# Kernel tuning notes

Hardware: AMD Instinct MI355X
Metric: run time of the kernel (lower is better)

## Reference

```python
import jax, jax.numpy as jnp
import numpy as np

B, N, D = 2, 2048, 1024
H = 16
HD = D // H  # head_dim for kq and v

def setup_inputs() -> dict:
    key = jax.random.key(0)
    ks = jax.random.split(key, 5)
    scale = 1.0 / np.sqrt(D)
    return {
        "x": jax.random.normal(ks[0], (B, N, D), dtype=jnp.float32),
        "Wq": jax.random.normal(ks[1], (D, D), dtype=jnp.float32) * scale,
        "Wk": jax.random.normal(ks[2], (D, D), dtype=jnp.float32) * scale,
        "Wv": jax.random.normal(ks[3], (D, D), dtype=jnp.float32) * scale,
        "Wo": jax.random.normal(ks[4], (D, D), dtype=jnp.float32) * scale,
        "bo": jnp.zeros((D,), dtype=jnp.float32),
    }

def reference(x, Wq, Wk, Wv, Wo, bo):
    b, n, _ = x.shape
    # projections; torch Linear computes x @ W.T
    q = (x @ Wq.T).reshape(b, n, H, HD).transpose(0, 2, 1, 3)  # [B,H,N,HD]
    k = (x @ Wk.T).reshape(b, n, H, HD).transpose(0, 2, 1, 3)
    v = (x @ Wv.T).reshape(b, n, H, HD).transpose(0, 2, 1, 3)
    scores = jnp.einsum('bhqd,bhkd->bhqk', q, k) / jnp.sqrt(jnp.asarray(HD, x.dtype))
    causal = jnp.tril(jnp.ones((n, n), dtype=bool))
    scores = jnp.where(causal, scores, jnp.asarray(-jnp.inf, scores.dtype))
    probs = jax.nn.softmax(scores, axis=-1)  # dropout p=0.0 (eval)
    out = jnp.einsum('bhqk,bhkd->bhqd', probs, v)  # [B,H,N,HD]
    out = out.transpose(0, 2, 1, 3).reshape(b, n, D)
    return out @ Wo.T + bo
```

## Files before the change

kernel.cpp:

```cpp
#include <hip/hip_runtime.h>
#include <hip/hip_bf16.h>


typedef __bf16 bf16;
typedef __bf16 bf16x2 __attribute__((ext_vector_type(2)));
typedef __bf16 bf16x4 __attribute__((ext_vector_type(4)));
typedef __bf16 bf16x8 __attribute__((ext_vector_type(8)));
typedef float f32x4 __attribute__((ext_vector_type(4)));
typedef unsigned int u32x4 __attribute__((ext_vector_type(4)));

__device__ __forceinline__ f32x4 mfma16(bf16x8 a, bf16x8 b, f32x4 c) {
    return __builtin_amdgcn_mfma_f32_16x16x32_bf16(a, b, c, 0, 0, 0);
}

__device__ __forceinline__ void gload16(const bf16* g, bf16* l) {
    __builtin_amdgcn_global_load_lds(
        (const __attribute__((address_space(1))) unsigned int*)g,
        (__attribute__((address_space(3))) unsigned int*)l, 16, 0, 0);
}

__device__ __forceinline__ unsigned pk2(float a, float b) {
    bf16x2 v;
    v[0] = (bf16)a;
    v[1] = (bf16)b;
    return __builtin_bit_cast(unsigned, v);
}

__global__ __launch_bounds__(256) void conv_kernel(
    const float* __restrict__ x, const float* __restrict__ w0,
    const float* __restrict__ w1, const float* __restrict__ w2,
    const float* __restrict__ w3, bf16* __restrict__ xb,
    bf16* __restrict__ o0, bf16* __restrict__ o1,
    bf16* __restrict__ o2, bf16* __restrict__ o3) {
    int blk = blockIdx.x;
    const float* in;
    bf16* out;
    int base;
    if (blk < 4096) {
        in = x; out = xb; base = blk;
    } else {
        int sel = (blk - 4096) >> 10;
        in = sel == 0 ? w0 : sel == 1 ? w1 : sel == 2 ? w2 : w3;
        out = sel == 0 ? o0 : sel == 1 ? o1 : sel == 2 ? o2 : o3;
        base = (blk - 4096) & 1023;
    }
    int i = (base * 256 + threadIdx.x) * 4;
    float4 v = *(const float4*)&in[i];
    bf16x4 o;
    o.x = (bf16)v.x; o.y = (bf16)v.y; o.z = (bf16)v.z; o.w = (bf16)v.w;
    *(bf16x4*)&out[i] = o;
}

template <int MODE>
__device__ __forceinline__ void gemm_body(bf16* __restrict__ sA, bf16* __restrict__ sB,
                                          const bf16* __restrict__ A,
                                          const bf16* __restrict__ B,
                                          bf16* __restrict__ Cb,
                                          float* __restrict__ Cf,
                                          const float* __restrict__ bias,
                                          float scale, int N, int K, int row0, int col0) {
    const int tid  = threadIdx.x;
    const int lane = tid & 63;
    const int wave = tid >> 6;
    const int wrow = (wave >> 1) * 64;
    const int wcol = (wave & 1) * 64;
    const int la = lane & 15, lb = lane >> 4;

    const f32x4 fzero = {0.f, 0.f, 0.f, 0.f};
    f32x4 acc[4][4];
#pragma unroll
    for (int m = 0; m < 4; ++m)
#pragma unroll
        for (int n = 0; n < 4; ++n) acc[m][n] = fzero;

    auto STAGE = [&](int k0, int buf) {
#pragma unroll
        for (int i = 0; i < 2; ++i) {
            int idx = i * 256 + tid;
            int r = idx >> 2, s = idx & 3;
            gload16(&A[(size_t)(row0 + r) * K + k0 + s * 8], &sA[buf * 4096 + idx * 8]);
            gload16(&B[(size_t)(col0 + r) * K + k0 + s * 8], &sB[buf * 4096 + idx * 8]);
        }
    };
    auto COMPUTE = [&](int buf) {
        bf16x8 af[4], bfv[4];
#pragma unroll
        for (int m = 0; m < 4; ++m)
            af[m] = *(const bf16x8*)&sA[buf * 4096 + (wrow + m * 16 + la) * 32 + lb * 8];
#pragma unroll
        for (int n = 0; n < 4; ++n)
            bfv[n] = *(const bf16x8*)&sB[buf * 4096 + (wcol + n * 16 + la) * 32 + lb * 8];
#pragma unroll
        for (int m = 0; m < 4; ++m)
#pragma unroll
            for (int n = 0; n < 4; ++n)
                acc[m][n] = mfma16(af[m], bfv[n], acc[m][n]);
    };

    STAGE(0, 0);
    __syncthreads();
    for (int k0 = 0; k0 < K; k0 += 64) {
        if (k0 + 32 < K) STAGE(k0 + 32, 1);
        COMPUTE(0);
        __syncthreads();
        if (k0 + 64 < K) STAGE(k0 + 64, 0);
        COMPUTE(1);
        __syncthreads();
    }
#pragma unroll
    for (int m = 0; m < 4; ++m)
#pragma unroll
        for (int n = 0; n < 4; ++n) {
            int col = col0 + wcol + n * 16 + la;
            if (MODE == 2) {
                int hh = col >> 6, hd = col & 63;
                int hc = hd >> 4, lav = hd & 15;
                int sp = row0 + wrow + m * 16 + lb * 4;
                int ktile = sp >> 6, k = sp & 63;
                int c = k >> 4, q = k & 15;
                size_t addr = (size_t)(ktile * 16 + hh) * 4096 +
                              (size_t)(((hc * 2 + (c >> 1)) * 16 + lav) * 32 +
                                       (q >> 2) * 8 + (c & 1) * 4);
                bf16x4 o4;
#pragma unroll
                for (int r = 0; r < 4; ++r) o4[r] = (bf16)acc[m][n][r];
                *(bf16x4*)&Cb[addr] = o4;
            } else if (MODE == 3) {
                int hh = col >> 6, hd = col & 63;
#pragma unroll
                for (int r = 0; r < 4; ++r) {
                    int row = row0 + wrow + m * 16 + lb * 4 + r;
                    int ktile = row >> 6, key = row & 63;
                    size_t addr = (size_t)(ktile * 16 + hh) * 4096 +
                                  (size_t)((((key >> 4) * 2 + (hd >> 5)) * 16 +
                                            (key & 15)) * 32 +
                                           ((hd >> 3) & 3) * 8 + (hd & 7));
                    Cb[addr] = (bf16)acc[m][n][r];
                }
            } else {
#pragma unroll
                for (int r = 0; r < 4; ++r) {
                    int row = row0 + wrow + m * 16 + lb * 4 + r;
                    if (MODE == 1)
                        Cf[(size_t)row * N + col] = acc[m][n][r] + bias[col];
                    else
                        Cb[(size_t)row * N + col] = (bf16)(acc[m][n][r] * scale);
                }
            }
        }
}

__global__ __launch_bounds__(256) void gemm_qkv_kernel(
    const bf16* __restrict__ xb, const bf16* __restrict__ wq,
    const bf16* __restrict__ wk, const bf16* __restrict__ wv,
    bf16* __restrict__ Q, bf16* __restrict__ Kf, bf16* __restrict__ Vf) {
    extern __shared__ char dyn[];
    bf16* sA = (bf16*)dyn;
    bf16* sB = (bf16*)(dyn + 16384);
    int z = blockIdx.z;
    if (z == 2) {
        gemm_body<2>(sA, sB, xb, wv, Vf, nullptr, nullptr, 1.f, 1024, 1024,
                     blockIdx.x * 128, blockIdx.y * 128);
    } else if (z == 1) {
        gemm_body<3>(sA, sB, xb, wk, Kf, nullptr, nullptr, 1.f, 1024, 1024,
                     blockIdx.x * 128, blockIdx.y * 128);
    } else {
        gemm_body<0>(sA, sB, xb, wq, Q, nullptr, nullptr, 0.1803368801111204f,
                     1024, 1024, blockIdx.x * 128, blockIdx.y * 128);
    }
}

__global__ __launch_bounds__(256) void gemm_out_kernel(
    const bf16* __restrict__ att, const bf16* __restrict__ wo,
    float* __restrict__ out, const float* __restrict__ bias) {
    extern __shared__ char dyn[];
    bf16* sA = (bf16*)dyn;
    bf16* sB = (bf16*)(dyn + 16384);
    gemm_body<1>(sA, sB, att, wo, nullptr, out, bias, 1.f, 1024, 1024,
                 blockIdx.x * 128, blockIdx.y * 128);
}

struct KF { bf16x8 f[4][2]; };

__global__ __launch_bounds__(256, 2) void attn_kernel(
    const bf16* __restrict__ Q, const bf16* __restrict__ Kf,
    const bf16* __restrict__ Vf, bf16* __restrict__ O) {
    const int lane = threadIdx.x & 63;
    const int wave = threadIdx.x >> 6;
    const int bid = blockIdx.x;
    const int bh = (bid & 7) * 4 + ((bid >> 3) & 3);
    const int slot = bid >> 5;
    const int qt = slot < 8 ? slot : 23 - slot;
    const int h = bh & 15;
    const int b = bh >> 4;
    const int q0w = qt * 128 + wave * 32;
    const int rowbase = b * 2048;
    const int la = lane & 15, lb = lane >> 4;
    const f32x4 fzero = {0.f, 0.f, 0.f, 0.f};
    const float C = 14.426950408889634f;
    const int colbase = h * 64;
    const int lane_off = la * 32 + lb * 8;
    const int TSTRIDE = 16 * 4096;

    bf16x8 aq[2][2];
#pragma unroll
    for (int mf = 0; mf < 2; ++mf) {
        const bf16* qp = &Q[(size_t)(rowbase + q0w + mf * 16 + la) * 1024 + colbase];
#pragma unroll
        for (int kc = 0; kc < 2; ++kc) aq[mf][kc] = *(const bf16x8*)(qp + kc * 32 + lb * 8);
    }

    bf16x8 bones;
#pragma unroll
    for (int j = 0; j < 8; ++j) bones[j] = (bf16)1.0f;

    f32x4 o[2][4], lacc[2];
#pragma unroll
    for (int mf = 0; mf < 2; ++mf) {
        lacc[mf] = fzero;
#pragma unroll
        for (int hc = 0; hc < 4; ++hc) o[mf][hc] = fzero;
    }

    const int nt = (q0w + 95) >> 6;

    const bf16* kbase = &Kf[(size_t)(b * 32 * 16 + h) * 4096 + lane_off + 2048];
    const bf16* vbase = &Vf[(size_t)(b * 32 * 16 + h) * 4096 + lane_off + 2048];

    KF ka, kb, va, vb;
#pragma unroll
    for (int ck = 0; ck < 4; ++ck) {
        ka.f[ck][0] = *(const bf16x8*)(kbase + (ck * 2 + 0) * 512 - 2048);
        ka.f[ck][1] = *(const bf16x8*)(kbase + (ck * 2 + 1) * 512 - 2048);
        va.f[ck][0] = *(const bf16x8*)(vbase + (ck * 2 + 0) * 512 - 2048);
        va.f[ck][1] = *(const bf16x8*)(vbase + (ck * 2 + 1) * 512 - 2048);
    }
    const bf16* kpf = kbase + (nt > 1 ? TSTRIDE : 0);
    const bf16* vpf = vbase + (nt > 1 ? TSTRIDE : 0);

    auto TILE = [&](int t, KF& kc, KF& kn, KF& vc, KF& vn) {
        const bool domask = (t == nt - 1);
#pragma unroll
        for (int ck = 0; ck < 4; ++ck) {
            kn.f[ck][0] = *(const bf16x8*)(kpf + (ck * 2 + 0) * 512 - 2048);
            kn.f[ck][1] = *(const bf16x8*)(kpf + (ck * 2 + 1) * 512 - 2048);
            vn.f[ck][0] = *(const bf16x8*)(vpf + (ck * 2 + 0) * 512 - 2048);
            vn.f[ck][1] = *(const bf16x8*)(vpf + (ck * 2 + 1) * 512 - 2048);
        }
        int adv = (t + 2 < nt) ? TSTRIDE : 0;
        kpf += adv;
        vpf += adv;
        f32x4 s[2][4];
#pragma unroll
        for (int mf = 0; mf < 2; ++mf)
#pragma unroll
            for (int ck = 0; ck < 4; ++ck) s[mf][ck] = fzero;
        __builtin_amdgcn_s_setprio(1);
#pragma unroll
        for (int ck = 0; ck < 4; ++ck)
#pragma unroll
            for (int mf = 0; mf < 2; ++mf) {
                s[mf][ck] = mfma16(kc.f[ck][0], aq[mf][0], s[mf][ck]);
                s[mf][ck] = mfma16(kc.f[ck][1], aq[mf][1], s[mf][ck]);
            }
        __builtin_amdgcn_s_setprio(0);
        if (domask) {
            const int k0 = t * 64;
#pragma unroll
            for (int mf = 0; mf < 2; ++mf) {
                int qrow = q0w + mf * 16 + la;
#pragma unroll
                for (int ck = 0; ck < 4; ++ck)
#pragma unroll
                    for (int r = 0; r < 4; ++r) {
                        int key = k0 + ck * 16 + lb * 4 + r;
                        if (key > qrow) s[mf][ck][r] = -1e30f;
                    }
            }
        }
        bf16x8 pa[2][2];
#pragma unroll
        for (int mf = 0; mf < 2; ++mf) {
            unsigned pk[4][2];
#pragma unroll
            for (int ck = 0; ck < 4; ++ck) {
                float p0 = __builtin_amdgcn_exp2f(s[mf][ck][0] - C);
                float p1 = __builtin_amdgcn_exp2f(s[mf][ck][1] - C);
                float p2 = __builtin_amdgcn_exp2f(s[mf][ck][2] - C);
                float p3 = __builtin_amdgcn_exp2f(s[mf][ck][3] - C);
                pk[ck][0] = pk2(p0, p1);
                pk[ck][1] = pk2(p2, p3);
            }
#pragma unroll
            for (int kc2 = 0; kc2 < 2; ++kc2) {
                u32x4 w;
                w.x = pk[kc2 * 2][0];
                w.y = pk[kc2 * 2][1];
                w.z = pk[kc2 * 2 + 1][0];
                w.w = pk[kc2 * 2 + 1][1];
                pa[mf][kc2] = __builtin_bit_cast(bf16x8, w);
            }
        }
        __builtin_amdgcn_s_setprio(1);
#pragma unroll
        for (int hc = 0; hc < 4; ++hc)
#pragma unroll
            for (int mf = 0; mf < 2; ++mf) {
                o[mf][hc] = mfma16(pa[mf][0], vc.f[hc][0], o[mf][hc]);
                o[mf][hc] = mfma16(pa[mf][1], vc.f[hc][1], o[mf][hc]);
            }
#pragma unroll
        for (int mf = 0; mf < 2; ++mf) {
            lacc[mf] = mfma16(pa[mf][0], bones, lacc[mf]);
            lacc[mf] = mfma16(pa[mf][1], bones, lacc[mf]);
        }
        __builtin_amdgcn_s_setprio(0);
    };

    int t = 0;
    for (; t + 2 <= nt; t += 2) {
        TILE(t, ka, kb, va, vb);
        TILE(t + 1, kb, ka, vb, va);
    }
    if (t < nt) TILE(t, ka, kb, va, vb);

#pragma unroll
    for (int mf = 0; mf < 2; ++mf)
#pragma unroll
        for (int hc = 0; hc < 4; ++hc)
#pragma unroll
            for (int r = 0; r < 4; ++r) {
                int qrow = q0w + mf * 16 + lb * 4 + r;
                O[(size_t)(rowbase + qrow) * 1024 + colbase + hc * 16 + la] =
                    (bf16)(o[mf][hc][r] / lacc[mf][r]);
            }
}

extern "C" void kernel_launch(void* const* d_in, const int* in_sizes, int n_in,
                              void* d_out, int out_size, void* d_ws, size_t ws_size,
                              hipStream_t stream) {
    const float* x  = (const float*)d_in[0];
    const float* Wq = (const float*)d_in[1];
    const float* Wk = (const float*)d_in[2];
    const float* Wv = (const float*)d_in[3];
    const float* Wo = (const float*)d_in[4];
    const float* bo = (const float*)d_in[5];
    float* out = (float*)d_out;

    char* ws = (char*)d_ws;
    const size_t MB = 1024 * 1024;
    bf16* xb  = (bf16*)(ws + (size_t)0);
    bf16* wqb = (bf16*)(ws + 8 * MB);
    bf16* wkb = (bf16*)(ws + 10 * MB);
    bf16* wvb = (bf16*)(ws + 12 * MB);
    bf16* wob = (bf16*)(ws + 14 * MB);
    bf16* Qb  = (bf16*)(ws + 16 * MB);
    bf16* Kf  = (bf16*)(ws + 24 * MB);
    bf16* Vf  = (bf16*)(ws + 40 * MB);
    bf16* Ab  = (bf16*)(ws + 56 * MB);

    conv_kernel<<<8192, 256, 0, stream>>>(x, Wq, Wk, Wv, Wo, xb, wqb, wkb, wvb, wob);

    gemm_qkv_kernel<<<dim3(32, 8, 3), 256, 32768, stream>>>(xb, wqb, wkb, wvb,
                                                            Qb, Kf, Vf);
    attn_kernel<<<512, 256, 0, stream>>>(Qb, Kf, Vf, Ab);
    gemm_out_kernel<<<dim3(32, 8), 256, 32768, stream>>>(Ab, wob, out, bo);
}
```

Baseline: 100.3 us.

## Software-pipeline attention loop: overlap QK of tile t with PV of tile t-1

Restructures the flash-attention inner loop so each step issues the QK^T MFMAs for tile t together with the PV MFMAs for the previous tile's probabilities, then computes exp/pack for tile t afterward. The intent is to hide the exp2/convert latency of the softmax stage behind independent matrix-core work within a wave. V loads are shifted one tile behind K loads to match. This costs extra registers for a second probability buffer and more complex prologue and epilogue handling.

```diff
diff --git a/kernel.cpp b/kernel.cpp
--- a/kernel.cpp
+++ b/kernel.cpp
@@ -227,102 +227,108 @@
     const bf16* kbase = &Kf[(size_t)(b * 32 * 16 + h) * 4096 + lane_off + 2048];
     const bf16* vbase = &Vf[(size_t)(b * 32 * 16 + h) * 4096 + lane_off + 2048];
 
-    KF ka, kb, va, vb;
+    KF kA, kB, vA, vB;
+    bf16x8 pA[2][2], pB[2][2];
 #pragma unroll
     for (int ck = 0; ck < 4; ++ck) {
-        ka.f[ck][0] = *(const bf16x8*)(kbase + (ck * 2 + 0) * 512 - 2048);
-        ka.f[ck][1] = *(const bf16x8*)(kbase + (ck * 2 + 1) * 512 - 2048);
-        va.f[ck][0] = *(const bf16x8*)(vbase + (ck * 2 + 0) * 512 - 2048);
-        va.f[ck][1] = *(const bf16x8*)(vbase + (ck * 2 + 1) * 512 - 2048);
+        kA.f[ck][0] = *(const bf16x8*)(kbase + (ck * 2 + 0) * 512 - 2048);
+        kA.f[ck][1] = *(const bf16x8*)(kbase + (ck * 2 + 1) * 512 - 2048);
     }
     const bf16* kpf = kbase + (nt > 1 ? TSTRIDE : 0);
-    const bf16* vpf = vbase + (nt > 1 ? TSTRIDE : 0);
-
-    auto TILE = [&](int t, KF& kc, KF& kn, KF& vc, KF& vn) {
-        const bool domask = (t == nt - 1);
-#pragma unroll
-        for (int ck = 0; ck < 4; ++ck) {
-            kn.f[ck][0] = *(const bf16x8*)(kpf + (ck * 2 + 0) * 512 - 2048);
-            kn.f[ck][1] = *(const bf16x8*)(kpf + (ck * 2 + 1) * 512 - 2048);
-            vn.f[ck][0] = *(const bf16x8*)(vpf + (ck * 2 + 0) * 512 - 2048);
-            vn.f[ck][1] = *(const bf16x8*)(vpf + (ck * 2 + 1) * 512 - 2048);
-        }
-        int adv = (t + 2 < nt) ? TSTRIDE : 0;
-        kpf += adv;
-        vpf += adv;
+    const bf16* vpf = vbase;
+
+    auto STEP = [&](int t, KF& kc, KF& kn, KF& vc, KF& vn,
+                    bf16x8 (&pp)[2][2], bf16x8 (&pc)[2][2]) {
+        const bool doQK = (t < nt);
+        const bool doPV = (t >= 1);
+        if (doQK) {
+#pragma unroll
+            for (int ck = 0; ck < 4; ++ck) {
+                kn.f[ck][0] = *(const bf16x8*)(kpf + (ck * 2 + 0) * 512 - 2048);
+                kn.f[ck][1] = *(const bf16x8*)(kpf + (ck * 2 + 1) * 512 - 2048);
+                vn.f[ck][0] = *(const bf16x8*)(vpf + (ck * 2 + 0) * 512 - 2048);
+                vn.f[ck][1] = *(const bf16x8*)(vpf + (ck * 2 + 1) * 512 - 2048);
+            }
+            kpf += (t + 2 < nt) ? TSTRIDE : 0;
+            vpf += (t + 1 < nt) ? TSTRIDE : 0;
+        }
         f32x4 s[2][4];
-#pragma unroll
-        for (int mf = 0; mf < 2; ++mf)
-#pragma unroll
-            for (int ck = 0; ck < 4; ++ck) s[mf][ck] = fzero;
         __builtin_amdgcn_s_setprio(1);
-#pragma unroll
-        for (int ck = 0; ck < 4; ++ck)
+        if (doQK) {
+#pragma unroll
+            for (int mf = 0; mf < 2; ++mf)
+#pragma unroll
+                for (int ck = 0; ck < 4; ++ck) s[mf][ck] = fzero;
+#pragma unroll
+            for (int ck = 0; ck < 4; ++ck)
+#pragma unroll
+                for (int mf = 0; mf < 2; ++mf) {
+                    s[mf][ck] = mfma16(kc.f[ck][0], aq[mf][0], s[mf][ck]);
+                    s[mf][ck] = mfma16(kc.f[ck][1], aq[mf][1], s[mf][ck]);
+                }
+        }
+        if (doPV) {
+#pragma unroll
+            for (int hc = 0; hc < 4; ++hc)
+#pragma unroll
+                for (int mf = 0; mf < 2; ++mf) {
+                    o[mf][hc] = mfma16(pp[mf][0], vc.f[hc][0], o[mf][hc]);
+                    o[mf][hc] = mfma16(pp[mf][1], vc.f[hc][1], o[mf][hc]);
+                }
 #pragma unroll
             for (int mf = 0; mf < 2; ++mf) {
-                s[mf][ck] = mfma16(kc.f[ck][0], aq[mf][0], s[mf][ck]);
-                s[mf][ck] = mfma16(kc.f[ck][1], aq[mf][1], s[mf][ck]);
-            }
+                lacc[mf] = mfma16(pp[mf][0], bones, lacc[mf]);
+                lacc[mf] = mfma16(pp[mf][1], bones, lacc[mf]);
+            }
+        }
         __builtin_amdgcn_s_setprio(0);
-        if (domask) {
-            const int k0 = t * 64;
+        if (doQK) {
+            if (t == nt - 1) {
+                const int k0 = t * 64;
+#pragma unroll
+                for (int mf = 0; mf < 2; ++mf) {
+                    int qrow = q0w + mf * 16 + la;
+#pragma unroll
+                    for (int ck = 0; ck < 4; ++ck)
+#pragma unroll
+                        for (int r = 0; r < 4; ++r) {
+                            int key = k0 + ck * 16 + lb * 4 + r;
+                            if (key > qrow) s[mf][ck][r] = -1e30f;
+                        }
+                }
+            }
 #pragma unroll
             for (int mf = 0; mf < 2; ++mf) {
-                int qrow = q0w + mf * 16 + la;
-#pragma unroll
-                for (int ck = 0; ck < 4; ++ck)
-#pragma unroll
-                    for (int r = 0; r < 4; ++r) {
-                        int key = k0 + ck * 16 + lb * 4 + r;
-                        if (key > qrow) s[mf][ck][r] = -1e30f;
-                    }
-            }
-        }
-        bf16x8 pa[2][2];
-#pragma unroll
-        for (int mf = 0; mf < 2; ++mf) {
-            unsigned pk[4][2];
-#pragma unroll
-            for (int ck = 0; ck < 4; ++ck) {
-                float p0 = __builtin_amdgcn_exp2f(s[mf][ck][0] - C);
-                float p1 = __builtin_amdgcn_exp2f(s[mf][ck][1] - C);
-                float p2 = __builtin_amdgcn_exp2f(s[mf][ck][2] - C);
-                float p3 = __builtin_amdgcn_exp2f(s[mf][ck][3] - C);
-                pk[ck][0] = pk2(p0, p1);
-                pk[ck][1] = pk2(p2, p3);
-            }
-#pragma unroll
-            for (int kc2 = 0; kc2 < 2; ++kc2) {
-                u32x4 w;
-                w.x = pk[kc2 * 2][0];
-                w.y = pk[kc2 * 2][1];
-                w.z = pk[kc2 * 2 + 1][0];
-                w.w = pk[kc2 * 2 + 1][1];
-                pa[mf][kc2] = __builtin_bit_cast(bf16x8, w);
-            }
-        }
-        __builtin_amdgcn_s_setprio(1);
-#pragma unroll
-        for (int hc = 0; hc < 4; ++hc)
-#pragma unroll
-            for (int mf = 0; mf < 2; ++mf) {
-                o[mf][hc] = mfma16(pa[mf][0], vc.f[hc][0], o[mf][hc]);
-                o[mf][hc] = mfma16(pa[mf][1], vc.f[hc][1], o[mf][hc]);
-            }
-#pragma unroll
-        for (int mf = 0; mf < 2; ++mf) {
-            lacc[mf] = mfma16(pa[mf][0], bones, lacc[mf]);
-            lacc[mf] = mfma16(pa[mf][1], bones, lacc[mf]);
-        }
-        __builtin_amdgcn_s_setprio(0);
+                unsigned pk[4][2];
+#pragma unroll
+                for (int ck = 0; ck < 4; ++ck) {
+                    float p0 = __builtin_amdgcn_exp2f(s[mf][ck][0] - C);
+                    float p1 = __builtin_amdgcn_exp2f(s[mf][ck][1] - C);
+                    float p2 = __builtin_amdgcn_exp2f(s[mf][ck][2] - C);
+                    float p3 = __builtin_amdgcn_exp2f(s[mf][ck][3] - C);
+                    pk[ck][0] = pk2(p0, p1);
+                    pk[ck][1] = pk2(p2, p3);
+                }
+#pragma unroll
+                for (int kc2 = 0; kc2 < 2; ++kc2) {
+                    u32x4 w;
+                    w.x = pk[kc2 * 2][0];
+                    w.y = pk[kc2 * 2][1];
+                    w.z = pk[kc2 * 2 + 1][0];
+                    w.w = pk[kc2 * 2 + 1][1];
+                    pc[mf][kc2] = __builtin_bit_cast(bf16x8, w);
+                }
+            }
+        }
     };
 
-    int t = 0;
-    for (; t + 2 <= nt; t += 2) {
-        TILE(t, ka, kb, va, vb);
-        TILE(t + 1, kb, ka, vb, va);
-    }
-    if (t < nt) TILE(t, ka, kb, va, vb);
+    STEP(0, kA, kB, vB, vA, pB, pA);
+    int t = 1;
+    for (; t + 1 <= nt; t += 2) {
+        STEP(t,     kB, kA, vA, vB, pA, pB);
+        STEP(t + 1, kA, kB, vB, vA, pB, pA);
+    }
+    if (t <= nt) STEP(t, kB, kA, vA, vB, pA, pB);
 
 #pragma unroll
     for (int mf = 0; mf < 2; ++mf)
```

Result: slower. 146.1 us (+45.7%).
